# Performance work log

Hardware: AMD Instinct MI355X
Metric: run time of the kernel (lower is better)

The kernel has to match this reference:

```python
import jax, jax.numpy as jnp
import numpy as np

HIDDEN = 640
NQ = 10      # query heads
NKV = 2      # kv heads
HD = HIDDEN // NQ   # 64
GROUPS = NQ // NKV  # 5
THETA = 500000.0
EPS = 1e-6


def rmsnorm(x, g):
    rms = jnp.sqrt(jnp.mean(x * x, axis=-1, keepdims=True) + EPS)
    return x / rms * g


def bitlinear(x, w, g):
    """RMSNorm + ternary weight / int8 activation fake-quant + GEMM + rescale."""
    x = rmsnorm(x, g)
    alpha = jnp.maximum(jnp.mean(jnp.abs(w)), 1e-10)
    w_q = jnp.clip(jnp.round(w / alpha), -1.0, 1.0)
    w_q = w + jax.lax.stop_gradient(w_q - w)            # STE
    gamma = jnp.maximum(jnp.max(jnp.abs(x), axis=-1, keepdims=True), 1e-10)
    x_q = jnp.clip(jnp.round(x * 127.0 / gamma), -128.0, 127.0)
    x_q = x + jax.lax.stop_gradient(x_q - x)            # STE
    return (x_q @ w_q.T) * (alpha * gamma / 127.0)


def rope_tables(L):
    # half-dim cos/sin tables [L, HD//2]; equivalent to the torch code's
    # repeat_interleave followed by [..., ::2] slicing.
    freqs = 1.0 / THETA ** (jnp.arange(0, HD, 2, dtype=jnp.float32) / HD)
    ang = jnp.arange(L, dtype=jnp.float32)[:, None] * freqs[None, :]
    return jnp.cos(ang), jnp.sin(ang)


def apply_rope(x, cos, sin):
    # x: [B,H,L,D]; cos/sin: [L,D/2] broadcast over B,H
    x1 = x[..., ::2]
    x2 = x[..., 1::2]
    o1 = x1 * cos - x2 * sin
    o2 = x2 * cos + x1 * sin
    return jnp.stack([o1, o2], axis=-1).reshape(x.shape)


def setup_inputs() -> dict:
    key = jax.random.key(0)
    ks = jax.random.split(key, 6)
    B, L = 32, 512
    x = jax.random.normal(ks[0], (B, L, HIDDEN), dtype=jnp.float32)
    s_h = 1.0 / np.sqrt(HIDDEN)
    q_w = jax.random.normal(ks[1], (NQ * HD, HIDDEN), dtype=jnp.float32) * s_h
    k_w = jax.random.normal(ks[2], (NKV * HD, HIDDEN), dtype=jnp.float32) * s_h
    v_w = jax.random.normal(ks[3], (NKV * HD, HIDDEN), dtype=jnp.float32) * s_h
    o_w = jax.random.normal(ks[4], (HIDDEN, NQ * HD), dtype=jnp.float32) * (1.0 / np.sqrt(NQ * HD))
    ones = jnp.ones((HIDDEN,), dtype=jnp.float32)
    return {
        "x": x,
        "norm_w": ones,
        "q_w": q_w, "q_g": ones,
        "k_w": k_w, "k_g": ones,
        "v_w": v_w, "v_g": ones,
        "o_w": o_w, "o_g": jnp.ones((NQ * HD,), dtype=jnp.float32),
    }


def reference(x, norm_w, q_w, q_g, k_w, k_g, v_w, v_g, o_w, o_g):
    B, L, _ = x.shape
    residual = x
    h = rmsnorm(x, norm_w)
    q = bitlinear(h, q_w, q_g).reshape(B, L, NQ, HD).transpose(0, 2, 1, 3)
    k = bitlinear(h, k_w, k_g).reshape(B, L, NKV, HD).transpose(0, 2, 1, 3)
    v = bitlinear(h, v_w, v_g).reshape(B, L, NKV, HD).transpose(0, 2, 1, 3)
    cos, sin = rope_tables(L)
    q = apply_rope(q, cos, sin)
    k = apply_rope(k, cos, sin)
    k = jnp.repeat(k, GROUPS, axis=1)   # [B,NQ,L,HD]
    v = jnp.repeat(v, GROUPS, axis=1)
    scale = 1.0 / np.sqrt(HD).astype(np.float32)
    attn = jnp.einsum("bhqd,bhkd->bhqk", q, k) * scale
    attn = jax.nn.softmax(attn, axis=-1)
    out = jnp.einsum("bhqk,bhkd->bhqd", attn, v)
    out = out.transpose(0, 2, 1, 3).reshape(B, L, NQ * HD)
    return bitlinear(out, o_w, o_g) + residual
```

## Files before the change

kernel.cpp:

```cpp
#include <hip/hip_runtime.h>
#include <math.h>
#include <stdint.h>

#define HIDDEN 640
#define NTOK   16384
#define LSEQ   512
#define BATCH  32
#define NQH    10
#define NKVH   2
#define HDIM   64
#define GROUPS 5

typedef int      int4v  __attribute__((ext_vector_type(4)));
typedef int      int16v __attribute__((ext_vector_type(16)));
typedef _Float16 f16x8  __attribute__((ext_vector_type(8)));
typedef _Float16 f16x2  __attribute__((ext_vector_type(2)));
typedef float    f32x4  __attribute__((ext_vector_type(4)));

__device__ __forceinline__ float wred_sum(float v){
  #pragma unroll
  for (int m=1;m<64;m<<=1) v += __shfl_xor(v,m);
  return v;
}
__device__ __forceinline__ float wred_max(float v){
  #pragma unroll
  for (int m=1;m<64;m<<=1) v = fmaxf(v,__shfl_xor(v,m));
  return v;
}

__device__ __forceinline__ int frag_flat(int m, int k){
  return (((m>>5)*20 + (k>>5))<<10) + (((((k>>4)&1)<<5) | (m&31))<<4) + (k&15);
}

__global__ __launch_bounds__(256) void absum4_kernel(
    const float* __restrict__ w0, const float* __restrict__ w1,
    const float* __restrict__ w2, const float* __restrict__ w3,
    float* __restrict__ sums){
  const float* w; int n;
  switch(blockIdx.y){
    case 0:  w=w0; n=640*640; break;
    case 1:  w=w1; n=128*640; break;
    case 2:  w=w2; n=128*640; break;
    default: w=w3; n=640*640; break;
  }
  __shared__ float red[256];
  int tid = threadIdx.x;
  float s = 0.f;
  for (int i = blockIdx.x*256 + tid; i < n; i += gridDim.x*256) s += fabsf(w[i]);
  red[tid] = s; __syncthreads();
  for (int off=128; off>0; off>>=1){ if (tid<off) red[tid]+=red[tid+off]; __syncthreads(); }
  if (tid==0) atomicAdd(&sums[blockIdx.y], red[0]);
}

__global__ __launch_bounds__(256) void wquant4_kernel(
    const float* __restrict__ w0, const float* __restrict__ w1,
    const float* __restrict__ w2, const float* __restrict__ w3,
    int8_t* __restrict__ o0, int8_t* __restrict__ o1,
    int8_t* __restrict__ o2, int8_t* __restrict__ o3,
    const float* __restrict__ sums){
  const float* w; int8_t* o; int n;
  switch(blockIdx.y){
    case 0:  w=w0; o=o0; n=640*640; break;
    case 1:  w=w1; o=o1; n=128*640; break;
    case 2:  w=w2; o=o2; n=128*640; break;
    default: w=w3; o=o3; n=640*640; break;
  }
  float alpha = fmaxf(sums[blockIdx.y]/(float)n, 1e-10f);
  float inva  = 1.0f/alpha;
  int i = blockIdx.x*256 + threadIdx.x;
  if (i < n){
    float t = rintf(w[i]*inva);
    t = fminf(1.f, fmaxf(-1.f, t));
    int nr = i/640;
    int kc = i - nr*640;
    o[frag_flat(nr, kc)] = (int8_t)t;
  }
}

__global__ __launch_bounds__(256) void token_prep_kernel(
    const float* __restrict__ x, const float* __restrict__ nw,
    const float* __restrict__ qg, const float* __restrict__ kg, const float* __restrict__ vg,
    int8_t* __restrict__ xqq, int8_t* __restrict__ xqk, int8_t* __restrict__ xqv,
    float* __restrict__ gq, float* __restrict__ gk, float* __restrict__ gv){
  int lane = threadIdx.x & 63;
  int m = blockIdx.x*4 + (threadIdx.x>>6);
  const float* xr = x + (size_t)m*HIDDEN;
  int abase = ((m>>5)*20480) + ((m&31)<<4)
            + ((lane>>5)<<10) + (((lane>>4)&1)<<9) + (lane&15);
  float xv[10], h[10];
  float ss = 0.f;
  #pragma unroll
  for (int j=0;j<10;j++){ float t = xr[lane + 64*j]; xv[j]=t; ss += t*t; }
  float inv1 = 1.0f/sqrtf(wred_sum(ss)*(1.0f/HIDDEN) + 1e-6f);
  float ss2 = 0.f;
  #pragma unroll
  for (int j=0;j<10;j++){ float t = xv[j]*inv1*nw[lane+64*j]; h[j]=t; ss2 += t*t; }
  float inv2 = 1.0f/sqrtf(wred_sum(ss2)*(1.0f/HIDDEN) + 1e-6f);

  const float* gs[3] = {qg, kg, vg};
  int8_t* outs[3] = {xqq, xqk, xqv};
  float* gams[3] = {gq, gk, gv};
  #pragma unroll
  for (int s=0;s<3;s++){
    const float* g = gs[s];
    float t[10], amax = 0.f;
    #pragma unroll
    for (int j=0;j<10;j++){ float v = h[j]*inv2*g[lane+64*j]; t[j]=v; amax = fmaxf(amax, fabsf(v)); }
    float gamma = fmaxf(wred_max(amax), 1e-10f);
    float sc = 127.0f/gamma;
    int8_t* dst = outs[s] + abase;
    #pragma unroll
    for (int j=0;j<10;j++){
      float v = rintf(t[j]*sc);
      v = fminf(127.f, fmaxf(-128.f, v));
      dst[j*2048] = (int8_t)v;
    }
    if (lane==0) gams[s][m] = gamma;
  }
}

__global__ __launch_bounds__(256) void o_prep_kernel(const _Float16* __restrict__ ao,
    const float* __restrict__ og, int8_t* __restrict__ xqo, float* __restrict__ go){
  int lane = threadIdx.x & 63;
  int m = blockIdx.x*4 + (threadIdx.x>>6);
  const _Float16* xr = ao + (size_t)m*HIDDEN;
  int abase = ((m>>5)*20480) + ((m&31)<<4)
            + ((lane>>5)<<10) + (((lane>>4)&1)<<9) + (lane&15);
  float xv[10];
  float ss = 0.f;
  #pragma unroll
  for (int j=0;j<10;j++){ float t = (float)xr[lane + 64*j]; xv[j]=t; ss += t*t; }
  float inv = 1.0f/sqrtf(wred_sum(ss)*(1.0f/HIDDEN) + 1e-6f);
  float t[10], amax = 0.f;
  #pragma unroll
  for (int j=0;j<10;j++){ float v = xv[j]*inv*og[lane+64*j]; t[j]=v; amax = fmaxf(amax, fabsf(v)); }
  float gamma = fmaxf(wred_max(amax), 1e-10f);
  float sc = 127.0f/gamma;
  int8_t* dst = xqo + abase;
  #pragma unroll
  for (int j=0;j<10;j++){
    float v = rintf(t[j]*sc);
    v = fminf(127.f, fmaxf(-128.f, v));
    dst[j*2048] = (int8_t)v;
  }
  if (lane==0) go[m] = gamma;
}

__device__ __forceinline__ void gemm_core(
    const int8_t* __restrict__ xq, const int8_t* __restrict__ wqf,
    int m0, int n0, int lane, int16v& acc0, int16v& acc1){
  const int8_t* a0 = xq  + (size_t)(m0>>5)*20480 + (lane<<4);
  const int8_t* b0 = wqf + (size_t)(n0>>5)*20480 + (lane<<4);
  const int8_t* b1 = b0 + 20480;
  #pragma unroll
  for (int kb=0; kb<20; kb++){
    int4v a  = *(const int4v*)(a0 + (kb<<10));
    int4v v0 = *(const int4v*)(b0 + (kb<<10));
    int4v v1 = *(const int4v*)(b1 + (kb<<10));
    acc0 = __builtin_amdgcn_mfma_i32_32x32x32_i8(a, v0, acc0, 0, 0, 0);
    acc1 = __builtin_amdgcn_mfma_i32_32x32x32_i8(a, v1, acc1, 0, 0, 0);
  }
}

__global__ __launch_bounds__(256) void qkv_gemm_kernel(
    const int8_t* __restrict__ xq_q, const float* __restrict__ g_q, const int8_t* __restrict__ wq_q,
    const int8_t* __restrict__ xq_k, const float* __restrict__ g_k, const int8_t* __restrict__ wq_k,
    const int8_t* __restrict__ xq_v, const float* __restrict__ g_v, const int8_t* __restrict__ wq_v,
    const float* __restrict__ sums,
    _Float16* __restrict__ qbuf, _Float16* __restrict__ kbuf, _Float16* __restrict__ vbuf){
  __shared__ _Float16 Tr[4][64][40];
  int bx = blockIdx.x;
  const int8_t *xq, *wq; const float* gam; _Float16* outh;
  int n0, aidx, nheads, mode; float inv_nw, vscale;
  if (bx < 10){ xq=xq_q; wq=wq_q; gam=g_q; outh=qbuf; n0=bx*64;      aidx=0; inv_nw=1.0f/409600.f; nheads=NQH;  mode=1; vscale=0.18033688011110918f; }
  else if (bx < 12){ xq=xq_k; wq=wq_k; gam=g_k; outh=kbuf; n0=(bx-10)*64; aidx=1; inv_nw=1.0f/81920.f; nheads=NKVH; mode=1; vscale=1.0f; }
  else { xq=xq_v; wq=wq_v; gam=g_v; outh=vbuf; n0=(bx-12)*64; aidx=2; inv_nw=1.0f/81920.f; nheads=NKVH; mode=2; vscale=1.0f; }

  int lane = threadIdx.x & 63;
  int w    = threadIdx.x >> 6;
  int m0   = blockIdx.y*128 + w*32;
  int half = lane >> 5, lan5 = lane & 31;

  int16v acc0 = {0}, acc1 = {0};
  gemm_core(xq, wq, m0, n0, lane, acc0, acc1);

  float alpha = fmaxf(sums[aidx]*inv_nw, 1e-10f);
  float fr0 = 0.f, fr1 = 0.f;
  if (mode == 1){
    int d0 = (lan5) & ~1;
    int d1 = (32 + lan5) & ~1;
    fr0 = __expf(-(float)d0*(1.0f/64.0f)*13.122363377404328f);
    fr1 = __expf(-(float)d1*(1.0f/64.0f)*13.122363377404328f);
  }

  #pragma unroll
  for (int reg=0; reg<16; reg++){
    int ml = (reg&3) + 8*(reg>>2) + 4*half;
    int m = m0 + ml;
    float sc = alpha*gam[m]*(1.0f/127.0f);
    float v0 = (float)acc0[reg]*sc;
    float v1 = (float)acc1[reg]*sc;
    if (mode == 1){
      int b = m >> 9, l = m & 511;
      int head = n0 >> 6;
      float p0 = __shfl_xor(v0, 1);
      float p1 = __shfl_xor(v1, 1);
      float sn0, cs0, sn1, cs1;
      __sincosf((float)l*fr0, &sn0, &cs0);
      __sincosf((float)l*fr1, &sn1, &cs1);
      if (lane & 1){ v0 = v0*cs0 + p0*sn0;  v1 = v1*cs1 + p1*sn1; }
      else         { v0 = v0*cs0 - p0*sn0;  v1 = v1*cs1 - p1*sn1; }
      _Float16* dst = outh + ((((size_t)b*nheads + head)*LSEQ + l)<<6);
      dst[lan5]      = (_Float16)(v0*vscale);
      dst[32 + lan5] = (_Float16)(v1*vscale);
    } else {
      Tr[w][lan5][ml]      = (_Float16)v0;
      Tr[w][32 + lan5][ml] = (_Float16)v1;
    }
  }
  if (mode == 2){
    int b = m0 >> 9, l0 = m0 & 511;
    int head = n0 >> 6;
    f16x8 r0 = *(const f16x8*)&Tr[w][lane][0];
    f16x8 r1 = *(const f16x8*)&Tr[w][lane][8];
    f16x8 r2 = *(const f16x8*)&Tr[w][lane][16];
    f16x8 r3 = *(const f16x8*)&Tr[w][lane][24];
    _Float16* dst = outh + (((size_t)b*nheads + head)*HDIM + lane)*LSEQ + l0;
    ((f16x8*)dst)[0] = r0;
    ((f16x8*)dst)[1] = r1;
    ((f16x8*)dst)[2] = r2;
    ((f16x8*)dst)[3] = r3;
  }
}

__global__ __launch_bounds__(256) void out_gemm_kernel(
    const int8_t* __restrict__ xq, const float* __restrict__ gam,
    const int8_t* __restrict__ wq, const float* __restrict__ sums,
    const float* __restrict__ resid, float* __restrict__ outf){
  int lane = threadIdx.x & 63;
  int w    = threadIdx.x >> 6;
  int m0   = blockIdx.y*128 + w*32;
  int n0   = blockIdx.x*64;
  int half = lane >> 5, lan5 = lane & 31;

  int16v acc0 = {0}, acc1 = {0};
  gemm_core(xq, wq, m0, n0, lane, acc0, acc1);

  float alpha = fmaxf(sums[3]*(1.0f/409600.f), 1e-10f);
  #pragma unroll
  for (int reg=0; reg<16; reg++){
    int m = m0 + (reg&3) + 8*(reg>>2) + 4*half;
    float sc = alpha*gam[m]*(1.0f/127.0f);
    size_t ofs = (size_t)m*HIDDEN;
    outf[ofs + n0 + lan5]      = (float)acc0[reg]*sc + resid[ofs + n0 + lan5];
    outf[ofs + n0 + 32 + lan5] = (float)acc1[reg]*sc + resid[ofs + n0 + 32 + lan5];
  }
}

__device__ __forceinline__ int kv_addr(int row, int chunk){
  return (row<<6) + (((chunk ^ (row&7)))<<3);
}

__device__ __forceinline__ void softmax_half(
    const f32x4* S, float& m, float& l, f32x4* O, int quad,
    f16x8& pf0, f16x8& pf1){
  float t0 = fmaxf(fmaxf(S[0][0],S[0][1]), fmaxf(S[0][2],S[0][3]));
  float t1 = fmaxf(fmaxf(S[1][0],S[1][1]), fmaxf(S[1][2],S[1][3]));
  float t2 = fmaxf(fmaxf(S[2][0],S[2][1]), fmaxf(S[2][2],S[2][3]));
  float t3 = fmaxf(fmaxf(S[3][0],S[3][1]), fmaxf(S[3][2],S[3][3]));
  float tmax = fmaxf(fmaxf(t0,t1), fmaxf(t2,t3));
  tmax = fmaxf(tmax, __shfl_xor(tmax, 16));
  tmax = fmaxf(tmax, __shfl_xor(tmax, 32));
  if (__any(tmax > m + 8.0f)){
    float mnew = fmaxf(m, tmax);
    float af = exp2f(m - mnew);
    m = mnew;
    l *= af;
    #pragma unroll
    for (int r=0;r<4;r++){
      float afr = __shfl(af, (quad<<2)+r);
      O[0][r]*=afr; O[1][r]*=afr; O[2][r]*=afr; O[3][r]*=afr;
    }
  }
  float ps = 0.f;
  uint32_t W[4][2];
  #pragma unroll
  for (int nt=0;nt<4;nt++){
    float p0 = exp2f(S[nt][0]-m);
    float p1 = exp2f(S[nt][1]-m);
    float p2 = exp2f(S[nt][2]-m);
    float p3 = exp2f(S[nt][3]-m);
    ps += (p0+p1)+(p2+p3);
    f16x2 w0 = {(_Float16)p0, (_Float16)p1};
    f16x2 w1 = {(_Float16)p2, (_Float16)p3};
    W[nt][0] = __builtin_bit_cast(uint32_t, w0);
    W[nt][1] = __builtin_bit_cast(uint32_t, w1);
  }
  ps += __shfl_xor(ps, 16);
  ps += __shfl_xor(ps, 32);
  l += ps;
  #pragma unroll
  for (int p=0;p<2;p++){
    asm volatile("v_permlane32_swap_b32 %0, %1" : "+v"(W[0][p]), "+v"(W[1][p]));
    asm volatile("v_permlane32_swap_b32 %0, %1" : "+v"(W[2][p]), "+v"(W[3][p]));
    asm volatile("v_permlane16_swap_b32 %0, %1" : "+v"(W[0][p]), "+v"(W[1][p]));
    asm volatile("v_permlane16_swap_b32 %0, %1" : "+v"(W[2][p]), "+v"(W[3][p]));
  }
  union { uint32_t u[4]; f16x8 v; } a, b;
  a.u[0]=W[0][0]; a.u[1]=W[0][1]; a.u[2]=W[1][0]; a.u[3]=W[1][1];
  b.u[0]=W[2][0]; b.u[1]=W[2][1]; b.u[2]=W[3][0]; b.u[3]=W[3][1];
  pf0 = a.v; pf1 = b.v;
}

__global__ __launch_bounds__(256,3) void attn_mfma_kernel(
    const _Float16* __restrict__ q, const _Float16* __restrict__ k,
    const _Float16* __restrict__ vt, _Float16* __restrict__ o){
  __shared__ _Float16 Ks[2][64*64];
  __shared__ _Float16 Vs[2][64*64];
  int tid  = threadIdx.x;
  int wv   = tid >> 6, lane = tid & 63;
  int quad = lane >> 4, c = lane & 15;
  int h = blockIdx.y, b = blockIdx.z;
  int hk = h / GROUPS;
  int qrow0 = blockIdx.x*128 + wv*32;
  (void)wv;

  const _Float16* qb = q + ((size_t)((b*NQH+h)*LSEQ) + qrow0 + c)*HDIM + quad*8;
  f16x8 qa0 = *(const f16x8*)qb;
  f16x8 qa1 = *(const f16x8*)(qb + 32);
  f16x8 qb0 = *(const f16x8*)(qb + 16*HDIM);
  f16x8 qb1 = *(const f16x8*)(qb + 16*HDIM + 32);

  const _Float16* kbase = k  + (size_t)((b*NKVH+hk)*LSEQ)*HDIM;
  const _Float16* vbase = vt + (size_t)((b*NKVH+hk)*HDIM)*LSEQ;

  int srow = tid >> 3, schunk = tid & 7;
  const _Float16* kg0 = kbase + (size_t)srow*HDIM      + schunk*8;
  const _Float16* kg1 = kbase + (size_t)(srow+32)*HDIM + schunk*8;
  const _Float16* vg0 = vbase + (size_t)srow*LSEQ      + schunk*8;
  const _Float16* vg1 = vbase + (size_t)(srow+32)*LSEQ + schunk*8;
  int ka0 = kv_addr(srow,    schunk);
  int ka1 = kv_addr(srow+32, schunk);

  {
    f16x8 t0 = *(const f16x8*)kg0;
    f16x8 t1 = *(const f16x8*)kg1;
    f16x8 t2 = *(const f16x8*)vg0;
    f16x8 t3 = *(const f16x8*)vg1;
    *(f16x8*)&Ks[0][ka0] = t0;
    *(f16x8*)&Ks[0][ka1] = t1;
    *(f16x8*)&Vs[0][ka0] = t2;
    *(f16x8*)&Vs[0][ka1] = t3;
  }

  f32x4 O0[4] = {{0,0,0,0},{0,0,0,0},{0,0,0,0},{0,0,0,0}};
  f32x4 O1[4] = {{0,0,0,0},{0,0,0,0},{0,0,0,0},{0,0,0,0}};
  float m0s = -INFINITY, m1s = -INFINITY;
  float l0s = 0.f, l1s = 0.f;
  f16x8 pk0, pk1, pv0, pv1;

  for (int kt=0; kt<8; kt++){
    __syncthreads();
    int cur = kt & 1, nxt = cur ^ 1;
    if (kt < 7){
      pk0 = *(const f16x8*)(kg0 + (size_t)(kt+1)*64*HDIM);
      pk1 = *(const f16x8*)(kg1 + (size_t)(kt+1)*64*HDIM);
      pv0 = *(const f16x8*)(vg0 + (kt+1)*64);
      pv1 = *(const f16x8*)(vg1 + (kt+1)*64);
    }
    f32x4 S0[4], S1[4];
    #pragma unroll
    for (int nt=0; nt<4; nt++){
      int row = (nt<<4) + c;
      f16x8 kf0 = *(const f16x8*)&Ks[cur][kv_addr(row, quad)];
      f16x8 kf1 = *(const f16x8*)&Ks[cur][kv_addr(row, quad+4)];
      f32x4 s = {0,0,0,0};
      s = __builtin_amdgcn_mfma_f32_16x16x32_f16(kf0, qa0, s, 0,0,0);
      s = __builtin_amdgcn_mfma_f32_16x16x32_f16(kf1, qa1, s, 0,0,0);
      S0[nt] = s;
      f32x4 s2 = {0,0,0,0};
      s2 = __builtin_amdgcn_mfma_f32_16x16x32_f16(kf0, qb0, s2, 0,0,0);
      s2 = __builtin_amdgcn_mfma_f32_16x16x32_f16(kf1, qb1, s2, 0,0,0);
      S1[nt] = s2;
    }
    f16x8 pf00, pf01, pf10, pf11;
    softmax_half(S0, m0s, l0s, O0, quad, pf00, pf01);
    softmax_half(S1, m1s, l1s, O1, quad, pf10, pf11);
    #pragma unroll
    for (int nt=0;nt<4;nt++){
      int row = (nt<<4) + c;
      f16x8 vf0 = *(const f16x8*)&Vs[cur][kv_addr(row, quad)];
      f16x8 vf1 = *(const f16x8*)&Vs[cur][kv_addr(row, quad+4)];
      O0[nt] = __builtin_amdgcn_mfma_f32_16x16x32_f16(pf00, vf0, O0[nt], 0,0,0);
      O0[nt] = __builtin_amdgcn_mfma_f32_16x16x32_f16(pf01, vf1, O0[nt], 0,0,0);
      O1[nt] = __builtin_amdgcn_mfma_f32_16x16x32_f16(pf10, vf0, O1[nt], 0,0,0);
      O1[nt] = __builtin_amdgcn_mfma_f32_16x16x32_f16(pf11, vf1, O1[nt], 0,0,0);
    }
    if (kt < 7){
      *(f16x8*)&Ks[nxt][ka0] = pk0;
      *(f16x8*)&Ks[nxt][ka1] = pk1;
      *(f16x8*)&Vs[nxt][ka0] = pv0;
      *(f16x8*)&Vs[nxt][ka1] = pv1;
    }
  }
  #pragma unroll
  for (int r=0;r<4;r++){
    float invl0 = 1.0f/__shfl(l0s, (quad<<2)+r);
    float invl1 = 1.0f/__shfl(l1s, (quad<<2)+r);
    int m0 = (b<<9) + qrow0 + (quad<<2) + r;
    _Float16* d0 = o + (size_t)m0*HIDDEN + (h<<6);
    _Float16* d1 = o + (size_t)(m0+16)*HIDDEN + (h<<6);
    #pragma unroll
    for (int nt=0;nt<4;nt++){
      d0[(nt<<4)+c] = (_Float16)(O0[nt][r]*invl0);
      d1[(nt<<4)+c] = (_Float16)(O1[nt][r]*invl1);
    }
  }
}

extern "C" void kernel_launch(void* const* d_in, const int* in_sizes, int n_in,
                              void* d_out, int out_size, void* d_ws, size_t ws_size,
                              hipStream_t stream){
  (void)in_sizes; (void)n_in; (void)out_size; (void)ws_size;
  const float* x  = (const float*)d_in[0];
  const float* nw = (const float*)d_in[1];
  const float* qw = (const float*)d_in[2];
  const float* qg = (const float*)d_in[3];
  const float* kw = (const float*)d_in[4];
  const float* kg = (const float*)d_in[5];
  const float* vw = (const float*)d_in[6];
  const float* vg = (const float*)d_in[7];
  const float* ow = (const float*)d_in[8];
  const float* og = (const float*)d_in[9];
  float* out = (float*)d_out;

  char* base = (char*)d_ws;
  size_t off = 0;
  auto alloc = [&](size_t nbytes)->void*{
    off = (off + 255) & ~(size_t)255;
    void* p = base + off;
    off += nbytes;
    return p;
  };
  float*  sums = (float*) alloc(4*sizeof(float));
  int8_t* wq_q = (int8_t*)alloc(640*640);
  int8_t* wq_k = (int8_t*)alloc(128*640);
  int8_t* wq_v = (int8_t*)alloc(128*640);
  int8_t* wq_o = (int8_t*)alloc(640*640);
  int8_t* xq_q = (int8_t*)alloc((size_t)NTOK*HIDDEN);
  int8_t* xq_k = (int8_t*)alloc((size_t)NTOK*HIDDEN);
  int8_t* xq_v = (int8_t*)alloc((size_t)NTOK*HIDDEN);
  int8_t* xq_o = (int8_t*)alloc((size_t)NTOK*HIDDEN);
  float*  g_q  = (float*) alloc((size_t)NTOK*4);
  float*  g_k  = (float*) alloc((size_t)NTOK*4);
  float*  g_v  = (float*) alloc((size_t)NTOK*4);
  float*  g_o  = (float*) alloc((size_t)NTOK*4);
  _Float16* qbuf = (_Float16*)alloc((size_t)BATCH*NQH *LSEQ*HDIM*2);
  _Float16* kbuf = (_Float16*)alloc((size_t)BATCH*NKVH*LSEQ*HDIM*2);
  _Float16* vbuf = (_Float16*)alloc((size_t)BATCH*NKVH*LSEQ*HDIM*2);
  _Float16* abuf = (_Float16*)alloc((size_t)NTOK*HIDDEN*2);

  (void)hipMemsetAsync(sums, 0, 4*sizeof(float), stream);
  absum4_kernel<<<dim3(64,4),256,0,stream>>>(qw, kw, vw, ow, sums);
  wquant4_kernel<<<dim3(1600,4),256,0,stream>>>(qw, kw, vw, ow, wq_q, wq_k, wq_v, wq_o, sums);

  token_prep_kernel<<<NTOK/4,256,0,stream>>>(x, nw, qg, kg, vg, xq_q, xq_k, xq_v, g_q, g_k, g_v);

  qkv_gemm_kernel<<<dim3(14,128),256,0,stream>>>(xq_q, g_q, wq_q,
                                                 xq_k, g_k, wq_k,
                                                 xq_v, g_v, wq_v,
                                                 sums, qbuf, kbuf, vbuf);

  attn_mfma_kernel<<<dim3(4,NQH,BATCH),256,0,stream>>>(qbuf, kbuf, vbuf, abuf);

  o_prep_kernel<<<NTOK/4,256,0,stream>>>(abuf, og, xq_o, g_o);
  out_gemm_kernel<<<dim3(10,128),256,0,stream>>>(xq_o, g_o, wq_o, sums, x, out);
}
```

Before: 238.5 us.

## Fold max subtraction into MFMA init and compute row sums via MFMA

The attention softmax now seeds the QK^T MFMA accumulator with the negated running max, so scores come out already shifted and the per-element subtraction disappears in the common no-rescale case. Row sums move from shuffle reductions to extra MFMAs against a ones vector, which leaves the sum in the same layout as O. Probabilities are packed with cvt_pkrtz, and s_setprio raises wave priority around the MFMA sections. This trades VALU and shuffle work for a few more MFMAs. The row sum now accumulates fp16-rounded probabilities instead of fp32 values, which slightly changes numerics.

```diff
diff --git a/kernel.cpp b/kernel.cpp
--- a/kernel.cpp
+++ b/kernel.cpp
@@ -262,7 +262,7 @@
 }
 
 __device__ __forceinline__ void softmax_half(
-    const f32x4* S, float& m, float& l, f32x4* O, int quad,
+    const f32x4* S, float& m, f32x4& lacc, f32x4* O, int quad, bool first,
     f16x8& pf0, f16x8& pf1){
   float t0 = fmaxf(fmaxf(S[0][0],S[0][1]), fmaxf(S[0][2],S[0][3]));
   float t1 = fmaxf(fmaxf(S[1][0],S[1][1]), fmaxf(S[1][2],S[1][3]));
@@ -271,40 +271,43 @@
   float tmax = fmaxf(fmaxf(t0,t1), fmaxf(t2,t3));
   tmax = fmaxf(tmax, __shfl_xor(tmax, 16));
   tmax = fmaxf(tmax, __shfl_xor(tmax, 32));
-  if (__any(tmax > m + 8.0f)){
-    float mnew = fmaxf(m, tmax);
-    float af = exp2f(m - mnew);
-    m = mnew;
-    l *= af;
+  float p[16];
+  if (first || __any(tmax > 8.0f)){
+    float delta = first ? tmax : fmaxf(tmax, 0.0f);
+    m += delta;
+    float af = exp2f(-delta);
     #pragma unroll
     for (int r=0;r<4;r++){
       float afr = __shfl(af, (quad<<2)+r);
+      lacc[r] *= afr;
       O[0][r]*=afr; O[1][r]*=afr; O[2][r]*=afr; O[3][r]*=afr;
     }
-  }
-  float ps = 0.f;
+    #pragma unroll
+    for (int nt=0;nt<4;nt++){
+      #pragma unroll
+      for (int j=0;j<4;j++) p[(nt<<2)+j] = exp2f(S[nt][j] - delta);
+    }
+  } else {
+    #pragma unroll
+    for (int nt=0;nt<4;nt++){
+      #pragma unroll
+      for (int j=0;j<4;j++) p[(nt<<2)+j] = exp2f(S[nt][j]);
+    }
+  }
   uint32_t W[4][2];
   #pragma unroll
   for (int nt=0;nt<4;nt++){
-    float p0 = exp2f(S[nt][0]-m);
-    float p1 = exp2f(S[nt][1]-m);
-    float p2 = exp2f(S[nt][2]-m);
-    float p3 = exp2f(S[nt][3]-m);
-    ps += (p0+p1)+(p2+p3);
-    f16x2 w0 = {(_Float16)p0, (_Float16)p1};
-    f16x2 w1 = {(_Float16)p2, (_Float16)p3};
-    W[nt][0] = __builtin_bit_cast(uint32_t, w0);
-    W[nt][1] = __builtin_bit_cast(uint32_t, w1);
-  }
-  ps += __shfl_xor(ps, 16);
-  ps += __shfl_xor(ps, 32);
-  l += ps;
-  #pragma unroll
-  for (int p=0;p<2;p++){
-    asm volatile("v_permlane32_swap_b32 %0, %1" : "+v"(W[0][p]), "+v"(W[1][p]));
-    asm volatile("v_permlane32_swap_b32 %0, %1" : "+v"(W[2][p]), "+v"(W[3][p]));
-    asm volatile("v_permlane16_swap_b32 %0, %1" : "+v"(W[0][p]), "+v"(W[1][p]));
-    asm volatile("v_permlane16_swap_b32 %0, %1" : "+v"(W[2][p]), "+v"(W[3][p]));
+    W[nt][0] = __builtin_bit_cast(uint32_t,
+                 __builtin_amdgcn_cvt_pkrtz(p[(nt<<2)+0], p[(nt<<2)+1]));
+    W[nt][1] = __builtin_bit_cast(uint32_t,
+                 __builtin_amdgcn_cvt_pkrtz(p[(nt<<2)+2], p[(nt<<2)+3]));
+  }
+  #pragma unroll
+  for (int pp=0;pp<2;pp++){
+    asm volatile("v_permlane32_swap_b32 %0, %1" : "+v"(W[0][pp]), "+v"(W[1][pp]));
+    asm volatile("v_permlane32_swap_b32 %0, %1" : "+v"(W[2][pp]), "+v"(W[3][pp]));
+    asm volatile("v_permlane16_swap_b32 %0, %1" : "+v"(W[0][pp]), "+v"(W[1][pp]));
+    asm volatile("v_permlane16_swap_b32 %0, %1" : "+v"(W[2][pp]), "+v"(W[3][pp]));
   }
   union { uint32_t u[4]; f16x8 v; } a, b;
   a.u[0]=W[0][0]; a.u[1]=W[0][1]; a.u[2]=W[1][0]; a.u[3]=W[1][1];
@@ -323,7 +326,6 @@
   int h = blockIdx.y, b = blockIdx.z;
   int hk = h / GROUPS;
   int qrow0 = blockIdx.x*128 + wv*32;
-  (void)wv;
 
   const _Float16* qb = q + ((size_t)((b*NQH+h)*LSEQ) + qrow0 + c)*HDIM + quad*8;
   f16x8 qa0 = *(const f16x8*)qb;
@@ -355,8 +357,10 @@
 
   f32x4 O0[4] = {{0,0,0,0},{0,0,0,0},{0,0,0,0},{0,0,0,0}};
   f32x4 O1[4] = {{0,0,0,0},{0,0,0,0},{0,0,0,0},{0,0,0,0}};
-  float m0s = -INFINITY, m1s = -INFINITY;
-  float l0s = 0.f, l1s = 0.f;
+  f32x4 lacc0 = {0,0,0,0}, lacc1 = {0,0,0,0};
+  float m0s = 0.f, m1s = 0.f;
+  const f16x8 ones = {(_Float16)1.f,(_Float16)1.f,(_Float16)1.f,(_Float16)1.f,
+                      (_Float16)1.f,(_Float16)1.f,(_Float16)1.f,(_Float16)1.f};
   f16x8 pk0, pk1, pv0, pv1;
 
   for (int kt=0; kt<8; kt++){
@@ -369,23 +373,30 @@
       pv1 = *(const f16x8*)(vg1 + (kt+1)*64);
     }
     f32x4 S0[4], S1[4];
+    __builtin_amdgcn_s_setprio(1);
     #pragma unroll
     for (int nt=0; nt<4; nt++){
       int row = (nt<<4) + c;
       f16x8 kf0 = *(const f16x8*)&Ks[cur][kv_addr(row, quad)];
       f16x8 kf1 = *(const f16x8*)&Ks[cur][kv_addr(row, quad+4)];
-      f32x4 s = {0,0,0,0};
+      f32x4 s = {-m0s,-m0s,-m0s,-m0s};
       s = __builtin_amdgcn_mfma_f32_16x16x32_f16(kf0, qa0, s, 0,0,0);
       s = __builtin_amdgcn_mfma_f32_16x16x32_f16(kf1, qa1, s, 0,0,0);
       S0[nt] = s;
-      f32x4 s2 = {0,0,0,0};
+      f32x4 s2 = {-m1s,-m1s,-m1s,-m1s};
       s2 = __builtin_amdgcn_mfma_f32_16x16x32_f16(kf0, qb0, s2, 0,0,0);
       s2 = __builtin_amdgcn_mfma_f32_16x16x32_f16(kf1, qb1, s2, 0,0,0);
       S1[nt] = s2;
     }
+    __builtin_amdgcn_s_setprio(0);
     f16x8 pf00, pf01, pf10, pf11;
-    softmax_half(S0, m0s, l0s, O0, quad, pf00, pf01);
-    softmax_half(S1, m1s, l1s, O1, quad, pf10, pf11);
+    softmax_half(S0, m0s, lacc0, O0, quad, kt==0, pf00, pf01);
+    softmax_half(S1, m1s, lacc1, O1, quad, kt==0, pf10, pf11);
+    __builtin_amdgcn_s_setprio(1);
+    lacc0 = __builtin_amdgcn_mfma_f32_16x16x32_f16(pf00, ones, lacc0, 0,0,0);
+    lacc0 = __builtin_amdgcn_mfma_f32_16x16x32_f16(pf01, ones, lacc0, 0,0,0);
+    lacc1 = __builtin_amdgcn_mfma_f32_16x16x32_f16(pf10, ones, lacc1, 0,0,0);
+    lacc1 = __builtin_amdgcn_mfma_f32_16x16x32_f16(pf11, ones, lacc1, 0,0,0);
     #pragma unroll
     for (int nt=0;nt<4;nt++){
       int row = (nt<<4) + c;
@@ -396,6 +407,7 @@
       O1[nt] = __builtin_amdgcn_mfma_f32_16x16x32_f16(pf10, vf0, O1[nt], 0,0,0);
       O1[nt] = __builtin_amdgcn_mfma_f32_16x16x32_f16(pf11, vf1, O1[nt], 0,0,0);
     }
+    __builtin_amdgcn_s_setprio(0);
     if (kt < 7){
       *(f16x8*)&Ks[nxt][ka0] = pk0;
       *(f16x8*)&Ks[nxt][ka1] = pk1;
@@ -405,8 +417,8 @@
   }
   #pragma unroll
   for (int r=0;r<4;r++){
-    float invl0 = 1.0f/__shfl(l0s, (quad<<2)+r);
-    float invl1 = 1.0f/__shfl(l1s, (quad<<2)+r);
+    float invl0 = 1.0f/lacc0[r];
+    float invl1 = 1.0f/lacc1[r];
     int m0 = (b<<9) + qrow0 + (quad<<2) + r;
     _Float16* d0 = o + (size_t)m0*HIDDEN + (h<<6);
     _Float16* d1 = o + (size_t)(m0+16)*HIDDEN + (h<<6);
```

New measurement: 238.2 us. No clear change (-0.1%).
